# Optimization experiments

Hardware: AMD Instinct MI355X
Metric: run time of the kernel (lower is better)

## Reference

```python
import jax, jax.numpy as jnp
import numpy as np

B, N, D = 4, 4096, 1024


def setup_inputs() -> dict:
    key = jax.random.key(0)
    ks = jax.random.split(key, 7)
    s = 1.0 / np.sqrt(D)
    return {
        "x": jax.random.normal(ks[0], (B, N, D), dtype=jnp.float32),
        "Wq": jax.random.uniform(ks[1], (D, D), jnp.float32, -s, s),
        "bq": jax.random.uniform(ks[2], (D,), jnp.float32, -s, s),
        "Wk": jax.random.uniform(ks[3], (D, D), jnp.float32, -s, s),
        "bk": jax.random.uniform(ks[4], (D,), jnp.float32, -s, s),
        "Wv": jax.random.uniform(ks[5], (D, D), jnp.float32, -s, s),
        "bv": jax.random.uniform(ks[6], (D,), jnp.float32, -s, s),
    }


def reference(x, Wq, bq, Wk, bk, Wv, bv):
    # Projections (nn.Linear: x @ W.T + b; here W stored as [in, out])
    Q = x @ Wq + bq
    K = x @ Wk + bk
    V = x @ Wv + bv
    Qp = jax.nn.elu(Q) + 1.0  # positive feature map
    Kp = jax.nn.elu(K) + 1.0
    KV = jnp.einsum('bnd,bne->bde', Kp, V)          # [B, D, D]
    numerator = jnp.einsum('bnd,bde->bne', Qp, KV)  # [B, N, D]
    K_sum = Kp.sum(axis=1)                           # [B, D]
    norm = jnp.einsum('bnd,bd->bn', Qp, K_sum)[..., None]
    eps = 1e-6
    return numerator / (norm + eps)
```

## Files before the change

### kernel.cpp

```cpp
#include <hip/hip_runtime.h>
#include <hip/hip_bf16.h>
#include <cstdint>

typedef __bf16 bf16x8 __attribute__((ext_vector_type(8)));
typedef float  f32x4  __attribute__((ext_vector_type(4)));
typedef unsigned short u16x8 __attribute__((ext_vector_type(8)));

__device__ __forceinline__ unsigned short f2bf(float f) {
  __hip_bfloat16 h = __float2bfloat16(f);
  return __builtin_bit_cast(unsigned short, h);
}
__device__ __forceinline__ float bf2f(unsigned short u) {
  return __builtin_bit_cast(float, (unsigned)u << 16);
}

#define GL2LDS16(gp, lp)                                                      \
  __builtin_amdgcn_global_load_lds(                                           \
      (const __attribute__((address_space(1))) unsigned int*)(gp),            \
      (__attribute__((address_space(3))) unsigned int*)(lp), 16, 0, 0)

#define SBAR                                                                  \
  {                                                                           \
    __builtin_amdgcn_s_barrier();                                             \
    __builtin_amdgcn_sched_barrier(0);                                        \
  }
#define WAITV(n)                                                              \
  {                                                                           \
    asm volatile("s_waitcnt vmcnt(" #n ")" ::: "memory");                     \
    __builtin_amdgcn_sched_barrier(0);                                        \
  }
#define WAITL0                                                                \
  {                                                                           \
    asm volatile("s_waitcnt lgkmcnt(0)" ::: "memory");                        \
    __builtin_amdgcn_sched_barrier(0);                                        \
  }

template <int MODE>
__global__ __launch_bounds__(512, 2) void gemm256(
    const unsigned short* __restrict__ A, long long lda, long long aOffZ,
    const unsigned short* __restrict__ B, long long ldb, long long bOffZ,
    void* __restrict__ C, long long ldc, long long cOffZ,
    const float* __restrict__ bias, const float* __restrict__ bias2,
    const float* __restrict__ norm, long long normOffZ, int K) {
  __shared__ __attribute__((aligned(16))) char lds[4 * 32768];
  const int t = threadIdx.x;
  const int wave = t >> 6, lane = t & 63;
  const int wm = wave >> 2, wn = wave & 3;
  const int fr = lane & 15, fq = lane >> 4;

  const int gx = gridDim.x, gy = gridDim.y;
  int flat = blockIdx.y * gx + blockIdx.x;
  const int total = gx * gy;
  if ((total & 7) == 0) flat = (flat & 7) * (total >> 3) + (flat >> 3);
  const int bx = flat % gx, by = flat / gx;
  const int m0 = by * 256, n0 = bx * 256;

  const long long z = blockIdx.z;
  long long aBase, bBase;
  if (MODE == 3) {
    const long long koff = (z & 3) * 4096 + (z >> 2) * 1024;
    aBase = koff;
    bBase = koff;
  } else {
    aBase = z * aOffZ;
    bBase = z * bOffZ;
  }
  const unsigned short* Az = A + aBase;
  const unsigned short* Bz = B + bBase;

  const unsigned short* gA[2];
  const unsigned short* gB[2];
#pragma unroll
  for (int c = 0; c < 2; ++c) {
    int d = c * 8192 + t * 16;
    int l = d ^ (((d >> 7) & 3) << 4);
    int row = l >> 6, kel = (l & 63) >> 1;
    gA[c] = Az + (long long)(m0 + row) * lda + kel;
    gB[c] = Bz + (long long)(n0 + row) * ldb + kel;
  }

  const int slotx = (fr >> 1) & 3;
  const int abase = wm * 8192 + fr * 64 + ((fq ^ slotx) << 4);
  const int bbase = 16384 + wn * 4096 + fr * 64 + ((fq ^ slotx) << 4);

  f32x4 acc[8][4];
#pragma unroll
  for (int i = 0; i < 8; ++i)
#pragma unroll
    for (int j = 0; j < 4; ++j) acc[i][j] = (f32x4){0.f, 0.f, 0.f, 0.f};

  const int NT = K >> 5;

  auto stage = [&](int tile) {
    const int k0 = tile << 5;
    char* bufp = lds + (tile & 3) * 32768;
#pragma unroll
    for (int c = 0; c < 2; ++c)
      GL2LDS16(gA[c] + k0, bufp + c * 8192 + wave * 1024);
#pragma unroll
    for (int c = 0; c < 2; ++c)
      GL2LDS16(gB[c] + k0, bufp + 16384 + c * 8192 + wave * 1024);
  };

  stage(0);
  stage(1);
  stage(2);
  WAITV(8);
  SBAR;

  bf16x8 av[4], bv[4];
  for (int tt = 0; tt < NT - 3; ++tt) {
    const char* bufp = lds + (tt & 3) * 32768;
#pragma unroll
    for (int i = 0; i < 4; ++i) {
      av[i] = *(const bf16x8*)(bufp + abase + i * 1024);
      bv[i] = *(const bf16x8*)(bufp + bbase + i * 1024);
    }
    stage(tt + 3);
    SBAR;
    WAITL0;
    __builtin_amdgcn_s_setprio(1);
#pragma unroll
    for (int mi = 0; mi < 4; ++mi)
#pragma unroll
      for (int ni = 0; ni < 4; ++ni)
        acc[mi][ni] = __builtin_amdgcn_mfma_f32_16x16x32_bf16(
            av[mi], bv[ni], acc[mi][ni], 0, 0, 0);
    __builtin_amdgcn_s_setprio(0);
    SBAR;
#pragma unroll
    for (int i = 0; i < 4; ++i)
      av[i] = *(const bf16x8*)(bufp + abase + 4096 + i * 1024);
    SBAR;
    WAITL0;
    __builtin_amdgcn_s_setprio(1);
#pragma unroll
    for (int mi = 0; mi < 4; ++mi)
#pragma unroll
      for (int ni = 0; ni < 4; ++ni)
        acc[4 + mi][ni] = __builtin_amdgcn_mfma_f32_16x16x32_bf16(
            av[mi], bv[ni], acc[4 + mi][ni], 0, 0, 0);
    __builtin_amdgcn_s_setprio(0);
    WAITV(8);
    SBAR;
  }

  WAITV(0);
  SBAR;
#pragma unroll
  for (int e = 0; e < 3; ++e) {
    const char* bufp = lds + ((NT - 3 + e) & 3) * 32768;
#pragma unroll
    for (int i = 0; i < 4; ++i) {
      av[i] = *(const bf16x8*)(bufp + abase + i * 1024);
      bv[i] = *(const bf16x8*)(bufp + bbase + i * 1024);
    }
#pragma unroll
    for (int mi = 0; mi < 4; ++mi)
#pragma unroll
      for (int ni = 0; ni < 4; ++ni)
        acc[mi][ni] = __builtin_amdgcn_mfma_f32_16x16x32_bf16(
            av[mi], bv[ni], acc[mi][ni], 0, 0, 0);
#pragma unroll
    for (int i = 0; i < 4; ++i)
      av[i] = *(const bf16x8*)(bufp + abase + 4096 + i * 1024);
#pragma unroll
    for (int mi = 0; mi < 4; ++mi)
#pragma unroll
      for (int ni = 0; ni < 4; ++ni)
        acc[4 + mi][ni] = __builtin_amdgcn_mfma_f32_16x16x32_bf16(
            av[mi], bv[ni], acc[4 + mi][ni], 0, 0, 0);
  }

  const float* nrmz = (MODE == 4) ? (norm + z * normOffZ) : nullptr;
  float* Cf = (float*)C + z * cOffZ;
  unsigned short* Cu = (unsigned short*)C + z * cOffZ;
  const bool lower = (m0 < 1024);
#pragma unroll
  for (int mi = 0; mi < 8; ++mi) {
    const int rbase = m0 + wm * 128 + mi * 16 + fq * 4;
    float rb[4], nv[4];
#pragma unroll
    for (int j = 0; j < 4; ++j) {
      if (MODE == 1)
        rb[j] = lower ? bias[rbase + j] : bias2[rbase - 1024 + j];
      if (MODE == 4) nv[j] = nrmz[rbase + j];
    }
#pragma unroll
    for (int ni = 0; ni < 4; ++ni) {
      const int c = n0 + wn * 64 + ni * 16 + fr;
      float cb = 0.f;
      if (MODE == 0) cb = bias[c];
#pragma unroll
      for (int j = 0; j < 4; ++j) {
        float v = acc[mi][ni][j];
        if (MODE == 0) v += cb;
        if (MODE == 1) v += rb[j];
        if (MODE == 0 || (MODE == 1 && lower))
          v = (v > 0.f) ? v + 1.f : __expf(v);
        const long long ci = (long long)(rbase + j) * ldc + c;
        if (MODE == 4)
          Cf[ci] = v / nv[j];
        else
          Cu[ci] = f2bf(v);
      }
    }
  }
}

__global__ __launch_bounds__(256) void reduce_kvt(
    const unsigned short* __restrict__ P, unsigned short* __restrict__ KVt) {
  const long long i = ((long long)blockIdx.x * 256 + threadIdx.x) * 8;
  const int b = (int)(i >> 20);
  const long long ed = i & ((1ll << 20) - 1);
  float s[8] = {0.f, 0.f, 0.f, 0.f, 0.f, 0.f, 0.f, 0.f};
#pragma unroll
  for (int ks = 0; ks < 4; ++ks) {
    u16x8 v = *(const u16x8*)(P + ((long long)(ks * 4 + b) << 20) + ed);
#pragma unroll
    for (int j = 0; j < 8; ++j) s[j] += bf2f(v[j]);
  }
  u16x8 o;
#pragma unroll
  for (int j = 0; j < 8; ++j) o[j] = f2bf(s[j]);
  *(u16x8*)(KVt + i) = o;
}

__global__ __launch_bounds__(256) void transpose_w(
    const float* __restrict__ W, unsigned short* __restrict__ WT) {
  __shared__ float tile[32][33];
  const int tx = threadIdx.x & 31, ty = threadIdx.x >> 5;
  const int i0 = blockIdx.y * 32, o0 = blockIdx.x * 32;
#pragma unroll
  for (int s = 0; s < 32; s += 8)
    tile[ty + s][tx] = W[(long long)(i0 + ty + s) * 1024 + o0 + tx];
  __syncthreads();
#pragma unroll
  for (int s = 0; s < 32; s += 8)
    WT[(long long)(o0 + ty + s) * 1024 + i0 + tx] = f2bf(tile[tx][ty + s]);
}

__global__ __launch_bounds__(256) void convert_x(
    const float4* __restrict__ in, uint2* __restrict__ out, int n4) {
  const int stride = gridDim.x * blockDim.x;
  for (int i = blockIdx.x * blockDim.x + threadIdx.x; i < n4; i += stride) {
    float4 v = in[i];
    uint2 o;
    o.x = (unsigned)f2bf(v.x) | ((unsigned)f2bf(v.y) << 16);
    o.y = (unsigned)f2bf(v.z) | ((unsigned)f2bf(v.w) << 16);
    out[i] = o;
  }
}

__global__ __launch_bounds__(256) void ksum_kernel(
    const unsigned short* __restrict__ KpT, float* __restrict__ Ksum) {
  const int gw = (blockIdx.x * 256 + threadIdx.x) >> 6;
  const int lane = threadIdx.x & 63;
  const int d = gw >> 2, b = gw & 3;
  const unsigned short* p = KpT + (long long)d * 16384 + b * 4096;
  float s = 0.f;
  for (int i = lane; i < 4096; i += 64) s += bf2f(p[i]);
#pragma unroll
  for (int o = 32; o > 0; o >>= 1) s += __shfl_down(s, o, 64);
  if (lane == 0) Ksum[b * 1024 + d] = s;
}

__global__ __launch_bounds__(256) void norm_kernel(
    const unsigned short* __restrict__ Qp, const float* __restrict__ Ksum,
    float* __restrict__ nrm) {
  const int gw = (blockIdx.x * 256 + threadIdx.x) >> 6;
  const int lane = threadIdx.x & 63;
  const int b = gw >> 12;
  const unsigned short* q = Qp + (long long)gw * 1024;
  const float* ks = Ksum + b * 1024;
  float s = 0.f;
  for (int i = lane; i < 1024; i += 64) s += bf2f(q[i]) * ks[i];
#pragma unroll
  for (int o = 32; o > 0; o >>= 1) s += __shfl_down(s, o, 64);
  if (lane == 0) nrm[gw] = s + 1e-6f;
}

extern "C" void kernel_launch(void* const* d_in, const int* in_sizes, int n_in,
                              void* d_out, int out_size, void* d_ws,
                              size_t ws_size, hipStream_t stream) {
  const float* x  = (const float*)d_in[0];
  const float* Wq = (const float*)d_in[1];
  const float* bq = (const float*)d_in[2];
  const float* Wk = (const float*)d_in[3];
  const float* bk = (const float*)d_in[4];
  const float* Wv = (const float*)d_in[5];
  const float* bv = (const float*)d_in[6];
  float* out = (float*)d_out;

  const size_t MN = 16384ull * 1024ull;
  char* w = (char*)d_ws;
  unsigned short* xb  = (unsigned short*)w;  w += MN * 2;
  unsigned short* WT  = (unsigned short*)w;  w += 3ull * 1024 * 1024 * 2;
  unsigned short* Qp  = (unsigned short*)w;  w += MN * 2;
  unsigned short* KVb = (unsigned short*)w;  w += 2 * MN * 2;
  unsigned short* KVt = (unsigned short*)w;  w += 4ull * 1024 * 1024 * 2;
  float* Ksum = (float*)w;  w += 4ull * 1024 * 4;
  float* nrm  = (float*)w;  w += 16384ull * 4;
  unsigned short* Pkv = xb;
  unsigned short* KpT = KVb;
  unsigned short* VT  = KVb + MN;

  transpose_w<<<dim3(32, 32), 256, 0, stream>>>(Wq, WT);
  transpose_w<<<dim3(32, 32), 256, 0, stream>>>(Wk, WT + 1024 * 1024);
  transpose_w<<<dim3(32, 32), 256, 0, stream>>>(Wv, WT + 2 * 1024 * 1024);
  convert_x<<<2048, 256, 0, stream>>>((const float4*)x, (uint2*)xb,
                                      (int)(MN / 4));

  gemm256<0><<<dim3(4, 64, 1), 512, 0, stream>>>(
      xb, 1024, 0, WT, 1024, 0, Qp, 1024, 0, bq, nullptr, nullptr, 0, 1024);
  gemm256<1><<<dim3(64, 8, 1), 512, 0, stream>>>(
      WT + 1024 * 1024, 1024, 0, xb, 1024, 0, KVb, 16384, 0, bk, bv, nullptr,
      0, 1024);
  ksum_kernel<<<1024, 256, 0, stream>>>(KpT, Ksum);
  gemm256<3><<<dim3(4, 4, 16), 512, 0, stream>>>(
      VT, 16384, 0, KpT, 16384, 0, Pkv, 1024, 1024 * 1024, nullptr, nullptr,
      nullptr, 0, 1024);
  reduce_kvt<<<2048, 256, 0, stream>>>(Pkv, KVt);
  norm_kernel<<<4096, 256, 0, stream>>>(Qp, Ksum, nrm);
  gemm256<4><<<dim3(4, 16, 4), 512, 0, stream>>>(
      Qp, 1024, 4096ll * 1024, KVt, 1024, 1024 * 1024, out, 1024,
      4096ll * 1024, nullptr, nullptr, nrm, 4096, 1024);
}
```

Baseline: 275.9 us.

## Fuse K-sum into K projection epilogue and merge MFMA phases

Removes the separate ksum kernel by accumulating the row sums of the Kp feature map in the MODE 1 GEMM epilogue, reducing across lanes with shuffles and then atomically adding into a Ksum buffer that is zeroed with a memset. The main GEMM loop now loads all eight A fragments up front and issues all 32 MFMAs in one block, dropping two barriers per K tile at the cost of more registers. MODE 1 also changes the block rasterization order. Sums are now taken from fp32 values before bf16 rounding, and the atomics make the accumulation order nondeterministic.

```diff
diff --git a/kernel.cpp b/kernel.cpp
--- a/kernel.cpp
+++ b/kernel.cpp
@@ -41,7 +41,8 @@
     const unsigned short* __restrict__ B, long long ldb, long long bOffZ,
     void* __restrict__ C, long long ldc, long long cOffZ,
     const float* __restrict__ bias, const float* __restrict__ bias2,
-    const float* __restrict__ norm, long long normOffZ, int K) {
+    const float* __restrict__ norm, long long normOffZ,
+    float* __restrict__ ksum, int K) {
   __shared__ __attribute__((aligned(16))) char lds[4 * 32768];
   const int t = threadIdx.x;
   const int wave = t >> 6, lane = t & 63;
@@ -52,7 +53,14 @@
   int flat = blockIdx.y * gx + blockIdx.x;
   const int total = gx * gy;
   if ((total & 7) == 0) flat = (flat & 7) * (total >> 3) + (flat >> 3);
-  const int bx = flat % gx, by = flat / gx;
+  int bx, by;
+  if (MODE == 1) {
+    bx = flat / gy;
+    by = flat - bx * gy;
+  } else {
+    bx = flat % gx;
+    by = flat / gx;
+  }
   const int m0 = by * 256, n0 = bx * 256;
 
   const long long z = blockIdx.z;
@@ -108,12 +116,13 @@
   WAITV(8);
   SBAR;
 
-  bf16x8 av[4], bv[4];
+  bf16x8 av[8], bv[4];
   for (int tt = 0; tt < NT - 3; ++tt) {
     const char* bufp = lds + (tt & 3) * 32768;
 #pragma unroll
     for (int i = 0; i < 4; ++i) {
       av[i] = *(const bf16x8*)(bufp + abase + i * 1024);
+      av[4 + i] = *(const bf16x8*)(bufp + abase + 4096 + i * 1024);
       bv[i] = *(const bf16x8*)(bufp + bbase + i * 1024);
     }
     stage(tt + 3);
@@ -121,26 +130,12 @@
     WAITL0;
     __builtin_amdgcn_s_setprio(1);
 #pragma unroll
-    for (int mi = 0; mi < 4; ++mi)
+    for (int mi = 0; mi < 8; ++mi)
 #pragma unroll
       for (int ni = 0; ni < 4; ++ni)
         acc[mi][ni] = __builtin_amdgcn_mfma_f32_16x16x32_bf16(
             av[mi], bv[ni], acc[mi][ni], 0, 0, 0);
     __builtin_amdgcn_s_setprio(0);
-    SBAR;
-#pragma unroll
-    for (int i = 0; i < 4; ++i)
-      av[i] = *(const bf16x8*)(bufp + abase + 4096 + i * 1024);
-    SBAR;
-    WAITL0;
-    __builtin_amdgcn_s_setprio(1);
-#pragma unroll
-    for (int mi = 0; mi < 4; ++mi)
-#pragma unroll
-      for (int ni = 0; ni < 4; ++ni)
-        acc[4 + mi][ni] = __builtin_amdgcn_mfma_f32_16x16x32_bf16(
-            av[mi], bv[ni], acc[4 + mi][ni], 0, 0, 0);
-    __builtin_amdgcn_s_setprio(0);
     WAITV(8);
     SBAR;
   }
@@ -153,38 +148,32 @@
 #pragma unroll
     for (int i = 0; i < 4; ++i) {
       av[i] = *(const bf16x8*)(bufp + abase + i * 1024);
+      av[4 + i] = *(const bf16x8*)(bufp + abase + 4096 + i * 1024);
       bv[i] = *(const bf16x8*)(bufp + bbase + i * 1024);
     }
 #pragma unroll
-    for (int mi = 0; mi < 4; ++mi)
+    for (int mi = 0; mi < 8; ++mi)
 #pragma unroll
       for (int ni = 0; ni < 4; ++ni)
         acc[mi][ni] = __builtin_amdgcn_mfma_f32_16x16x32_bf16(
             av[mi], bv[ni], acc[mi][ni], 0, 0, 0);
-#pragma unroll
-    for (int i = 0; i < 4; ++i)
-      av[i] = *(const bf16x8*)(bufp + abase + 4096 + i * 1024);
-#pragma unroll
-    for (int mi = 0; mi < 4; ++mi)
-#pragma unroll
-      for (int ni = 0; ni < 4; ++ni)
-        acc[4 + mi][ni] = __builtin_amdgcn_mfma_f32_16x16x32_bf16(
-            av[mi], bv[ni], acc[4 + mi][ni], 0, 0, 0);
   }
 
   const float* nrmz = (MODE == 4) ? (norm + z * normOffZ) : nullptr;
   float* Cf = (float*)C + z * cOffZ;
   unsigned short* Cu = (unsigned short*)C + z * cOffZ;
   const bool lower = (m0 < 1024);
+  const int bidx = n0 >> 12;
 #pragma unroll
   for (int mi = 0; mi < 8; ++mi) {
     const int rbase = m0 + wm * 128 + mi * 16 + fq * 4;
-    float rb[4], nv[4];
+    float rb[4], nv[4], ks[4];
 #pragma unroll
     for (int j = 0; j < 4; ++j) {
       if (MODE == 1)
         rb[j] = lower ? bias[rbase + j] : bias2[rbase - 1024 + j];
       if (MODE == 4) nv[j] = nrmz[rbase + j];
+      ks[j] = 0.f;
     }
 #pragma unroll
     for (int ni = 0; ni < 4; ++ni) {
@@ -198,11 +187,23 @@
         if (MODE == 1) v += rb[j];
         if (MODE == 0 || (MODE == 1 && lower))
           v = (v > 0.f) ? v + 1.f : __expf(v);
+        if (MODE == 1 && lower) ks[j] += v;
         const long long ci = (long long)(rbase + j) * ldc + c;
         if (MODE == 4)
           Cf[ci] = v / nv[j];
         else
           Cu[ci] = f2bf(v);
+      }
+    }
+    if (MODE == 1 && lower) {
+#pragma unroll
+      for (int j = 0; j < 4; ++j) {
+        float s = ks[j];
+        s += __shfl_xor(s, 1, 16);
+        s += __shfl_xor(s, 2, 16);
+        s += __shfl_xor(s, 4, 16);
+        s += __shfl_xor(s, 8, 16);
+        if (fr == 0) atomicAdd(&ksum[bidx * 1024 + rbase + j], s);
       }
     }
   }
@@ -250,19 +251,6 @@
     o.y = (unsigned)f2bf(v.z) | ((unsigned)f2bf(v.w) << 16);
     out[i] = o;
   }
-}
-
-__global__ __launch_bounds__(256) void ksum_kernel(
-    const unsigned short* __restrict__ KpT, float* __restrict__ Ksum) {
-  const int gw = (blockIdx.x * 256 + threadIdx.x) >> 6;
-  const int lane = threadIdx.x & 63;
-  const int d = gw >> 2, b = gw & 3;
-  const unsigned short* p = KpT + (long long)d * 16384 + b * 4096;
-  float s = 0.f;
-  for (int i = lane; i < 4096; i += 64) s += bf2f(p[i]);
-#pragma unroll
-  for (int o = 32; o > 0; o >>= 1) s += __shfl_down(s, o, 64);
-  if (lane == 0) Ksum[b * 1024 + d] = s;
 }
 
 __global__ __launch_bounds__(256) void norm_kernel(
@@ -305,6 +293,7 @@
   unsigned short* KpT = KVb;
   unsigned short* VT  = KVb + MN;
 
+  hipMemsetAsync(Ksum, 0, 4096 * sizeof(float), stream);
   transpose_w<<<dim3(32, 32), 256, 0, stream>>>(Wq, WT);
   transpose_w<<<dim3(32, 32), 256, 0, stream>>>(Wk, WT + 1024 * 1024);
   transpose_w<<<dim3(32, 32), 256, 0, stream>>>(Wv, WT + 2 * 1024 * 1024);
@@ -312,17 +301,17 @@
                                       (int)(MN / 4));
 
   gemm256<0><<<dim3(4, 64, 1), 512, 0, stream>>>(
-      xb, 1024, 0, WT, 1024, 0, Qp, 1024, 0, bq, nullptr, nullptr, 0, 1024);
+      xb, 1024, 0, WT, 1024, 0, Qp, 1024, 0, bq, nullptr, nullptr, 0, nullptr,
+      1024);
   gemm256<1><<<dim3(64, 8, 1), 512, 0, stream>>>(
       WT + 1024 * 1024, 1024, 0, xb, 1024, 0, KVb, 16384, 0, bk, bv, nullptr,
-      0, 1024);
-  ksum_kernel<<<1024, 256, 0, stream>>>(KpT, Ksum);
+      0, Ksum, 1024);
   gemm256<3><<<dim3(4, 4, 16), 512, 0, stream>>>(
       VT, 16384, 0, KpT, 16384, 0, Pkv, 1024, 1024 * 1024, nullptr, nullptr,
-      nullptr, 0, 1024);
+      nullptr, 0, nullptr, 1024);
   reduce_kvt<<<2048, 256, 0, stream>>>(Pkv, KVt);
   norm_kernel<<<4096, 256, 0, stream>>>(Qp, Ksum, nrm);
   gemm256<4><<<dim3(4, 16, 4), 512, 0, stream>>>(
       Qp, 1024, 4096ll * 1024, KVt, 1024, 1024 * 1024, out, 1024,
-      4096ll * 1024, nullptr, nullptr, nrm, 4096, 1024);
-}
+      4096ll * 1024, nullptr, nullptr, nrm, 4096, nullptr, 1024);
+}
```

New measurement: 271.6 us. No clear change (-1.6%).
